# Optimization experiments

Measured on AMD Instinct MI355X. Metric: run time of the kernel, lower is better.

## Reference

```python
import jax, jax.numpy as jnp
import numpy as np
import math

DIM = 1024
B, S = 4, 2048

def setup_inputs() -> dict:
    key = jax.random.key(0)
    ks = jax.random.split(key, 4)
    scale = 1.0 / math.sqrt(DIM)
    X = jax.random.normal(ks[0], (B, S, DIM), dtype=jnp.float32)
    W_in = jax.random.normal(ks[1], (3 * DIM, DIM), dtype=jnp.float32) * scale
    b_in = jnp.zeros((3 * DIM,), dtype=jnp.float32)
    W_out = jax.random.normal(ks[2], (DIM, DIM), dtype=jnp.float32) * scale
    b_out = jnp.zeros((DIM,), dtype=jnp.float32)
    attention_mask = jnp.ones((B, 1, S), dtype=jnp.int32)
    return {"X": X, "attention_mask": attention_mask, "W_in": W_in,
            "b_in": b_in, "W_out": W_out, "b_out": b_out}

def reference(X, attention_mask, W_in, b_in, W_out, b_out):
    # in_proj: [B,S,3*DIM]
    qkv = jnp.einsum('bsd,ed->bse', X, W_in) + b_in
    Q, K, V = jnp.split(qkv, 3, axis=-1)
    # scores: [B,S,S]
    scores = jnp.einsum('bqd,bkd->bqk', Q, K)
    # masked_fill happens BEFORE the /sqrt(dim) scaling in the original
    scores = jnp.where(attention_mask == 0, jnp.float32(-1e20), scores)
    attn = jax.nn.softmax(scores / jnp.float32(math.sqrt(DIM)), axis=-1)
    # Dropout(0.1) treated as identity (eval-mode reference)
    out = jnp.einsum('bqk,bkd->bqd', attn, V)
    return jnp.einsum('bsd,od->bso', out, W_out) + b_out
```

## Files before the change

### kernel.cpp

```cpp
#include <hip/hip_runtime.h>
#include <stdint.h>

#define AS1 __attribute__((address_space(1)))
#define AS3 __attribute__((address_space(3)))

typedef __bf16 bf16x8 __attribute__((ext_vector_type(8)));
typedef float f32x16 __attribute__((ext_vector_type(16)));

__device__ __forceinline__ unsigned short f2bf(float f) {
  unsigned u = __float_as_uint(f);
  u += 0x7FFF + ((u >> 16) & 1);
  return (unsigned short)(u >> 16);
}
__device__ __forceinline__ float bf2f(unsigned short h) {
  return __uint_as_float(((unsigned)h) << 16);
}

__global__ __launch_bounds__(256) void cast_all_kernel(const float* __restrict__ X,
                                                       const float* __restrict__ Wi,
                                                       const float* __restrict__ Wo,
                                                       unsigned short* __restrict__ out) {
  const int c1 = 2097152;
  const int c2 = 786432;
  const int c3 = 262144;
  int i = blockIdx.x * 256 + threadIdx.x;
  if (i >= c1 + c2 + c3) return;
  const float* src;
  int j = i;
  if (i < c1) src = X;
  else if (i < c1 + c2) { src = Wi; j = i - c1; }
  else { src = Wo; j = i - c1 - c2; }
  float4 v = reinterpret_cast<const float4*>(src)[j];
  ushort4 o;
  o.x = f2bf(v.x); o.y = f2bf(v.y); o.z = f2bf(v.z); o.w = f2bf(v.w);
  reinterpret_cast<ushort4*>(out)[i] = o;
}

template<int OUT_BF16>
__global__ __launch_bounds__(256, 2) void gemm_bt128(
    const unsigned short* __restrict__ A, long lda, long strideA,
    const unsigned short* __restrict__ B, long ldb, long strideB,
    void* __restrict__ Cv, long ldc, long strideC,
    const float* __restrict__ bias, const int* __restrict__ mask, int K) {
  __shared__ unsigned short sA[128 * 64];
  __shared__ unsigned short sB[128 * 64];
  const int t = threadIdx.x;
  const int lane = t & 63;
  const int wave = t >> 6;

  const unsigned short* Ab = A + (size_t)blockIdx.z * strideA + (size_t)blockIdx.y * 128 * lda;
  const unsigned short* Bb = B + (size_t)blockIdx.z * strideB + (size_t)blockIdx.x * 128 * ldb;

  const int srow = t >> 3;
  const int schunk = (t & 7) ^ (srow & 7);
  const unsigned short* aptr = Ab + (size_t)srow * lda + schunk * 8;
  const unsigned short* bptr = Bb + (size_t)srow * ldb + schunk * 8;
  char* ldsA0 = (char*)&sA[0] + wave * 1024;
  char* ldsB0 = (char*)&sB[0] + wave * 1024;

  f32x16 acc[2][2];
#pragma unroll
  for (int i = 0; i < 2; i++)
#pragma unroll
    for (int j = 0; j < 2; j++)
#pragma unroll
      for (int r = 0; r < 16; r++) acc[i][j][r] = 0.f;

  const int wm = (wave >> 1) * 64;
  const int wn = (wave & 1) * 64;
  const int r31 = lane & 31;
  const int half = lane >> 5;
  const int swz = r31 & 7;

  int offA[2][4], offB[2][4];
#pragma unroll
  for (int i = 0; i < 2; i++)
#pragma unroll
    for (int s = 0; s < 4; s++) {
      offA[i][s] = (wm + i * 32 + r31) * 128 + (((2 * s + half) ^ swz) * 16);
      offB[i][s] = (wn + i * 32 + r31) * 128 + (((2 * s + half) ^ swz) * 16);
    }

  for (int k0 = 0; k0 < K; k0 += 64) {
    __syncthreads();
#pragma unroll
    for (int o = 0; o < 4; o++) {
      __builtin_amdgcn_global_load_lds((AS1 void*)(aptr + (size_t)o * 32 * lda + k0),
                                       (AS3 void*)(ldsA0 + o * 4096), 16, 0, 0);
      __builtin_amdgcn_global_load_lds((AS1 void*)(bptr + (size_t)o * 32 * ldb + k0),
                                       (AS3 void*)(ldsB0 + o * 4096), 16, 0, 0);
    }
    __syncthreads();
#pragma unroll
    for (int s = 0; s < 4; s++) {
      bf16x8 af[2], bfv[2];
#pragma unroll
      for (int i = 0; i < 2; i++) {
        af[i]  = *reinterpret_cast<const bf16x8*>((const char*)sA + offA[i][s]);
        bfv[i] = *reinterpret_cast<const bf16x8*>((const char*)sB + offB[i][s]);
      }
#pragma unroll
      for (int i = 0; i < 2; i++)
#pragma unroll
        for (int j = 0; j < 2; j++)
          acc[i][j] = __builtin_amdgcn_mfma_f32_32x32x16_bf16(af[i], bfv[j], acc[i][j], 0, 0, 0);
    }
  }

  const int* mrow = mask ? (mask + (size_t)blockIdx.z * 2048) : nullptr;
#pragma unroll
  for (int i = 0; i < 2; i++) {
    int gmb = blockIdx.y * 128 + wm + i * 32;
#pragma unroll
    for (int j = 0; j < 2; j++) {
      int gn = blockIdx.x * 128 + wn + j * 32 + r31;
      float bv = bias ? bias[gn] : 0.0f;
      bool msk = mrow ? (mrow[gn] == 0) : false;
#pragma unroll
      for (int r = 0; r < 16; r++) {
        int row = (r & 3) + 8 * (r >> 2) + 4 * half;
        float val = acc[i][j][r] + bv;
        if (msk) val = -1e20f;
        size_t off = (size_t)blockIdx.z * strideC + (size_t)(gmb + row) * ldc + gn;
        if (OUT_BF16)
          ((unsigned short*)Cv)[off] = f2bf(val);
        else
          ((float*)Cv)[off] = val;
      }
    }
  }
}

__global__ __launch_bounds__(256) void transpose_v(const unsigned short* __restrict__ qkv,
                                                   unsigned short* __restrict__ vt) {
  __shared__ unsigned short tile[64][68];
  int t = threadIdx.x;
  int s0 = blockIdx.x * 64, d0 = blockIdx.y * 64, b = blockIdx.z;
  const unsigned short* V = qkv + (size_t)b * 2048 * 3072 + 2048;
  unsigned short* Vt = vt + (size_t)b * 1024 * 2048;
  int r = t >> 4, c = (t & 15) * 4;
#pragma unroll
  for (int i = 0; i < 4; i++) {
    int s = r + i * 16;
    ushort4 v4 = *reinterpret_cast<const ushort4*>(&V[(size_t)(s0 + s) * 3072 + d0 + c]);
    tile[s][c] = v4.x; tile[s][c + 1] = v4.y; tile[s][c + 2] = v4.z; tile[s][c + 3] = v4.w;
  }
  __syncthreads();
#pragma unroll
  for (int i = 0; i < 4; i++) {
    int d = r + i * 16;
    ushort4 o;
    o.x = tile[c][d]; o.y = tile[c + 1][d]; o.z = tile[c + 2][d]; o.w = tile[c + 3][d];
    *reinterpret_cast<ushort4*>(&Vt[(size_t)(d0 + d) * 2048 + s0 + c]) = o;
  }
}

__global__ __launch_bounds__(256) void softmax_kernel(unsigned short* __restrict__ P) {
  const int S = 2048;
  int row = blockIdx.x * 4 + (threadIdx.x >> 6);
  int lane = threadIdx.x & 63;
  unsigned short* prow = P + (size_t)row * S;
  uint4 raw[4];
#pragma unroll
  for (int j = 0; j < 4; j++)
    raw[j] = reinterpret_cast<const uint4*>(prow)[lane + j * 64];
  float v[32];
  float mx = -3.4e38f;
#pragma unroll
  for (int j = 0; j < 4; j++) {
    const unsigned* pw = (const unsigned*)&raw[j];
#pragma unroll
    for (int h = 0; h < 4; h++) {
      float a = bf2f(pw[h] & 0xffff) * 0.03125f;
      float b = bf2f(pw[h] >> 16) * 0.03125f;
      v[j * 8 + h * 2] = a;
      v[j * 8 + h * 2 + 1] = b;
      mx = fmaxf(mx, fmaxf(a, b));
    }
  }
#pragma unroll
  for (int o = 32; o >= 1; o >>= 1) mx = fmaxf(mx, __shfl_xor(mx, o, 64));
  float s = 0.f;
#pragma unroll
  for (int e = 0; e < 32; e++) { v[e] = __expf(v[e] - mx); s += v[e]; }
#pragma unroll
  for (int o = 32; o >= 1; o >>= 1) s += __shfl_xor(s, o, 64);
  float inv = 1.0f / s;
#pragma unroll
  for (int j = 0; j < 4; j++) {
    uint4 o4;
    unsigned* ow = (unsigned*)&o4;
#pragma unroll
    for (int h = 0; h < 4; h++)
      ow[h] = f2bf(v[j * 8 + h * 2] * inv) |
              ((unsigned)f2bf(v[j * 8 + h * 2 + 1] * inv) << 16);
    reinterpret_cast<uint4*>(prow)[lane + j * 64] = o4;
  }
}

extern "C" void kernel_launch(void* const* d_in, const int* in_sizes, int n_in,
                              void* d_out, int out_size, void* d_ws, size_t ws_size,
                              hipStream_t stream) {
  const float* X = (const float*)d_in[0];
  const int* mask = (const int*)d_in[1];
  const float* W_in = (const float*)d_in[2];
  const float* b_in = (const float*)d_in[3];
  const float* W_out = (const float*)d_in[4];
  const float* b_out = (const float*)d_in[5];
  float* out = (float*)d_out;

  const int S = 2048, D = 1024;
  char* w = (char*)d_ws;
  unsigned short* Xb  = (unsigned short*)w;
  unsigned short* Wib = (unsigned short*)(w + 16777216);
  unsigned short* Wob = (unsigned short*)(w + 16777216 + 6291456);
  unsigned short* QKV = (unsigned short*)(w + 16777216 + 6291456 + 2097152);
  unsigned short* P   = (unsigned short*)(w + 16777216 + 6291456 + 2097152 + 50331648);
  unsigned short* Vt  = (unsigned short*)(w + 16777216 + 6291456 + 2097152 + 50331648 + 33554432);
  unsigned short* Ob  = Xb;

  cast_all_kernel<<<12288, 256, 0, stream>>>(X, W_in, W_out, Xb);

  gemm_bt128<1><<<dim3(24, 64, 1), 256, 0, stream>>>(Xb, D, 0, Wib, D, 0,
                                                     QKV, 3 * D, 0, b_in, nullptr, D);
  transpose_v<<<dim3(32, 16, 4), 256, 0, stream>>>(QKV, Vt);
  gemm_bt128<1><<<dim3(16, 16, 4), 256, 0, stream>>>(QKV, 3 * D, (long)S * 3 * D,
                                                     QKV + D, 3 * D, (long)S * 3 * D,
                                                     P, S, (long)S * S, nullptr, mask, D);
  softmax_kernel<<<2048, 256, 0, stream>>>(P);
  gemm_bt128<1><<<dim3(8, 16, 4), 256, 0, stream>>>(P, S, (long)S * S,
                                                    Vt, S, (long)D * S,
                                                    Ob, D, (long)S * D, nullptr, nullptr, S);
  gemm_bt128<0><<<dim3(8, 64, 1), 256, 0, stream>>>(Ob, D, 0, Wob, D, 0,
                                                    out, D, 0, b_out, nullptr, D);
}
```

Measured before the change: 301.2 us.

## Fuse V transpose, softmax exp, and normalization into GEMM epilogues

```diff
diff --git a/kernel.cpp b/kernel.cpp
--- a/kernel.cpp
+++ b/kernel.cpp
@@ -36,12 +36,13 @@
   reinterpret_cast<ushort4*>(out)[i] = o;
 }
 
-template<int OUT_BF16>
+template<int MODE>
 __global__ __launch_bounds__(256, 2) void gemm_bt128(
     const unsigned short* __restrict__ A, long lda, long strideA,
     const unsigned short* __restrict__ B, long ldb, long strideB,
     void* __restrict__ Cv, long ldc, long strideC,
-    const float* __restrict__ bias, const int* __restrict__ mask, int K) {
+    const float* __restrict__ bias, const int* __restrict__ mask,
+    const float* __restrict__ sums, unsigned short* __restrict__ vt, int K) {
   __shared__ unsigned short sA[128 * 64];
   __shared__ unsigned short sB[128 * 64];
   const int t = threadIdx.x;
@@ -107,95 +108,78 @@
     }
   }
 
-  const int* mrow = mask ? (mask + (size_t)blockIdx.z * 2048) : nullptr;
+  const int* mrow = (MODE == 2) ? (mask + (size_t)blockIdx.z * 2048) : nullptr;
+  const bool vblock = (MODE == 1) && (blockIdx.x >= 16);
+
 #pragma unroll
   for (int i = 0; i < 2; i++) {
     int gmb = blockIdx.y * 128 + wm + i * 32;
+    float inv_r[16];
+    if (MODE == 3) {
+#pragma unroll
+      for (int r = 0; r < 16; r++) {
+        int row = (r & 3) + 8 * (r >> 2) + 4 * half;
+        inv_r[r] = 1.0f / sums[(size_t)blockIdx.z * 2048 + gmb + row];
+      }
+    }
 #pragma unroll
     for (int j = 0; j < 2; j++) {
       int gn = blockIdx.x * 128 + wn + j * 32 + r31;
-      float bv = bias ? bias[gn] : 0.0f;
-      bool msk = mrow ? (mrow[gn] == 0) : false;
-#pragma unroll
-      for (int r = 0; r < 16; r++) {
-        int row = (r & 3) + 8 * (r >> 2) + 4 * half;
-        float val = acc[i][j][r] + bv;
-        if (msk) val = -1e20f;
-        size_t off = (size_t)blockIdx.z * strideC + (size_t)(gmb + row) * ldc + gn;
-        if (OUT_BF16)
-          ((unsigned short*)Cv)[off] = f2bf(val);
-        else
-          ((float*)Cv)[off] = val;
+      float bv = (MODE == 0 || MODE == 1) ? bias[gn] : 0.0f;
+      if (MODE == 1 && vblock) {
+        int b = gmb >> 11;
+        int sbase = gmb & 2047;
+        int d = gn - 2048;
+        unsigned short* vp = vt + (size_t)b * 1024 * 2048 + (size_t)d * 2048 + sbase + 4 * half;
+#pragma unroll
+        for (int qd = 0; qd < 4; qd++) {
+          ushort4 o;
+          o.x = f2bf(acc[i][j][4 * qd + 0] + bv);
+          o.y = f2bf(acc[i][j][4 * qd + 1] + bv);
+          o.z = f2bf(acc[i][j][4 * qd + 2] + bv);
+          o.w = f2bf(acc[i][j][4 * qd + 3] + bv);
+          *reinterpret_cast<ushort4*>(vp + 8 * qd) = o;
+        }
+      } else {
+        bool msk = (MODE == 2) ? (mrow[gn] == 0) : false;
+#pragma unroll
+        for (int r = 0; r < 16; r++) {
+          int row = (r & 3) + 8 * (r >> 2) + 4 * half;
+          float val = acc[i][j][r] + bv;
+          size_t off = (size_t)blockIdx.z * strideC + (size_t)(gmb + row) * ldc + gn;
+          if (MODE == 2) {
+            if (msk) val = -1e20f;
+            val = __expf(val * 0.03125f);
+            ((unsigned short*)Cv)[off] = f2bf(val);
+          } else if (MODE == 3) {
+            ((unsigned short*)Cv)[off] = f2bf(val * inv_r[r]);
+          } else if (MODE == 1) {
+            ((unsigned short*)Cv)[off] = f2bf(val);
+          } else {
+            ((float*)Cv)[off] = val;
+          }
+        }
       }
     }
   }
 }
 
-__global__ __launch_bounds__(256) void transpose_v(const unsigned short* __restrict__ qkv,
-                                                   unsigned short* __restrict__ vt) {
-  __shared__ unsigned short tile[64][68];
-  int t = threadIdx.x;
-  int s0 = blockIdx.x * 64, d0 = blockIdx.y * 64, b = blockIdx.z;
-  const unsigned short* V = qkv + (size_t)b * 2048 * 3072 + 2048;
-  unsigned short* Vt = vt + (size_t)b * 1024 * 2048;
-  int r = t >> 4, c = (t & 15) * 4;
-#pragma unroll
-  for (int i = 0; i < 4; i++) {
-    int s = r + i * 16;
-    ushort4 v4 = *reinterpret_cast<const ushort4*>(&V[(size_t)(s0 + s) * 3072 + d0 + c]);
-    tile[s][c] = v4.x; tile[s][c + 1] = v4.y; tile[s][c + 2] = v4.z; tile[s][c + 3] = v4.w;
-  }
-  __syncthreads();
-#pragma unroll
-  for (int i = 0; i < 4; i++) {
-    int d = r + i * 16;
-    ushort4 o;
-    o.x = tile[c][d]; o.y = tile[c + 1][d]; o.z = tile[c + 2][d]; o.w = tile[c + 3][d];
-    *reinterpret_cast<ushort4*>(&Vt[(size_t)(d0 + d) * 2048 + s0 + c]) = o;
-  }
-}
-
-__global__ __launch_bounds__(256) void softmax_kernel(unsigned short* __restrict__ P) {
-  const int S = 2048;
+__global__ __launch_bounds__(256) void rowsum_kernel(const unsigned short* __restrict__ P,
+                                                     float* __restrict__ sums) {
   int row = blockIdx.x * 4 + (threadIdx.x >> 6);
   int lane = threadIdx.x & 63;
-  unsigned short* prow = P + (size_t)row * S;
-  uint4 raw[4];
-#pragma unroll
-  for (int j = 0; j < 4; j++)
-    raw[j] = reinterpret_cast<const uint4*>(prow)[lane + j * 64];
-  float v[32];
-  float mx = -3.4e38f;
+  const uint4* pr = reinterpret_cast<const uint4*>(P + (size_t)row * 2048);
+  float s = 0.f;
 #pragma unroll
   for (int j = 0; j < 4; j++) {
-    const unsigned* pw = (const unsigned*)&raw[j];
-#pragma unroll
-    for (int h = 0; h < 4; h++) {
-      float a = bf2f(pw[h] & 0xffff) * 0.03125f;
-      float b = bf2f(pw[h] >> 16) * 0.03125f;
-      v[j * 8 + h * 2] = a;
-      v[j * 8 + h * 2 + 1] = b;
-      mx = fmaxf(mx, fmaxf(a, b));
-    }
+    uint4 raw = pr[lane + j * 64];
+    const unsigned* pw = (const unsigned*)&raw;
+#pragma unroll
+    for (int h = 0; h < 4; h++) { s += bf2f(pw[h] & 0xffff) + bf2f(pw[h] >> 16); }
   }
 #pragma unroll
-  for (int o = 32; o >= 1; o >>= 1) mx = fmaxf(mx, __shfl_xor(mx, o, 64));
-  float s = 0.f;
-#pragma unroll
-  for (int e = 0; e < 32; e++) { v[e] = __expf(v[e] - mx); s += v[e]; }
-#pragma unroll
   for (int o = 32; o >= 1; o >>= 1) s += __shfl_xor(s, o, 64);
-  float inv = 1.0f / s;
-#pragma unroll
-  for (int j = 0; j < 4; j++) {
-    uint4 o4;
-    unsigned* ow = (unsigned*)&o4;
-#pragma unroll
-    for (int h = 0; h < 4; h++)
-      ow[h] = f2bf(v[j * 8 + h * 2] * inv) |
-              ((unsigned)f2bf(v[j * 8 + h * 2 + 1] * inv) << 16);
-    reinterpret_cast<uint4*>(prow)[lane + j * 64] = o4;
-  }
+  if (lane == 0) sums[row] = s;
 }
 
 extern "C" void kernel_launch(void* const* d_in, const int* in_sizes, int n_in,
@@ -214,23 +198,23 @@
   unsigned short* Xb  = (unsigned short*)w;
   unsigned short* Wib = (unsigned short*)(w + 16777216);
   unsigned short* Wob = (unsigned short*)(w + 16777216 + 6291456);
-  unsigned short* QKV = (unsigned short*)(w + 16777216 + 6291456 + 2097152);
-  unsigned short* P   = (unsigned short*)(w + 16777216 + 6291456 + 2097152 + 50331648);
-  unsigned short* Vt  = (unsigned short*)(w + 16777216 + 6291456 + 2097152 + 50331648 + 33554432);
+  unsigned short* QK  = (unsigned short*)(w + 25165824);
+  unsigned short* P   = (unsigned short*)(w + 58720256);
+  unsigned short* Vt  = (unsigned short*)(w + 92274688);
+  float*          sums = (float*)(w + 109051904);
   unsigned short* Ob  = Xb;
 
   cast_all_kernel<<<12288, 256, 0, stream>>>(X, W_in, W_out, Xb);
 
-  gemm_bt128<1><<<dim3(24, 64, 1), 256, 0, stream>>>(Xb, D, 0, Wib, D, 0,
-                                                     QKV, 3 * D, 0, b_in, nullptr, D);
-  transpose_v<<<dim3(32, 16, 4), 256, 0, stream>>>(QKV, Vt);
-  gemm_bt128<1><<<dim3(16, 16, 4), 256, 0, stream>>>(QKV, 3 * D, (long)S * 3 * D,
-                                                     QKV + D, 3 * D, (long)S * 3 * D,
-                                                     P, S, (long)S * S, nullptr, mask, D);
-  softmax_kernel<<<2048, 256, 0, stream>>>(P);
-  gemm_bt128<1><<<dim3(8, 16, 4), 256, 0, stream>>>(P, S, (long)S * S,
-                                                    Vt, S, (long)D * S,
-                                                    Ob, D, (long)S * D, nullptr, nullptr, S);
-  gemm_bt128<0><<<dim3(8, 64, 1), 256, 0, stream>>>(Ob, D, 0, Wob, D, 0,
-                                                    out, D, 0, b_out, nullptr, D);
-}
+  gemm_bt128<1><<<dim3(24, 64, 1), 256, 0, stream>>>(
+      Xb, D, 0, Wib, D, 0, QK, 2048, 0, b_in, nullptr, nullptr, Vt, D);
+  gemm_bt128<2><<<dim3(16, 16, 4), 256, 0, stream>>>(
+      QK, 2048, (long)S * 2048, QK + 1024, 2048, (long)S * 2048,
+      P, S, (long)S * S, nullptr, mask, nullptr, nullptr, D);
+  rowsum_kernel<<<2048, 256, 0, stream>>>(P, sums);
+  gemm_bt128<3><<<dim3(8, 16, 4), 256, 0, stream>>>(
+      P, S, (long)S * S, Vt, S, (long)D * S,
+      Ob, D, (long)S * D, nullptr, nullptr, sums, nullptr, S);
+  gemm_bt128<0><<<dim3(8, 64, 1), 256, 0, stream>>>(
+      Ob, D, 0, Wob, D, 0, out, D, 0, b_out, nullptr, nullptr, nullptr, D);
+}
```

Result: no change. 300.9 us (-0.1%).
